# Kernel optimization log

Measured on AMD Instinct MI355X. Metric: run time of the kernel, lower is better.

The kernel has to match this reference:

```python
import jax, jax.numpy as jnp
import numpy as np

N_NODES = 100000


def gcn_conv(x, W, b, src, dst, n_nodes):
    # PyG GCNConv: h = x @ W; add self-loops; symmetric normalization
    # out_i = sum_{j in N(i) U {i}} deg_i^{-1/2} deg_j^{-1/2} h_j + b
    h = x @ W                                   # [N, F_out]
    # append self-loops
    loop = jnp.arange(n_nodes, dtype=src.dtype)
    s = jnp.concatenate([src, loop])            # [E+N]
    d = jnp.concatenate([dst, loop])            # [E+N]
    deg = jax.ops.segment_sum(jnp.ones_like(d, dtype=h.dtype), d,
                              num_segments=n_nodes)   # [N]
    dinv = jnp.where(deg > 0, jax.lax.rsqrt(deg), 0.0)
    norm = dinv[s] * dinv[d]                    # [E+N]
    msg = h[s] * norm[:, None]                  # [E+N, F_out]
    out = jax.ops.segment_sum(msg, d, num_segments=n_nodes)
    return out + b


def setup_inputs() -> dict:
    key = jax.random.key(0)
    k1, k2, k3, k4 = jax.random.split(key, 4)
    input_dim, hidden_dim, num_classes = 128, 64, 40
    n_edges = 1600000
    x = jax.random.normal(k1, (N_NODES, input_dim), dtype=jnp.float32)
    edge_index = jax.random.randint(k2, (2, n_edges), 0, N_NODES, dtype=jnp.int64)
    # Glorot-style init for the two GCNConv layers
    W1 = jax.random.normal(k3, (input_dim, hidden_dim), dtype=jnp.float32) / np.sqrt(input_dim)
    b1 = jnp.zeros((hidden_dim,), dtype=jnp.float32)
    W2 = jax.random.normal(k4, (hidden_dim, num_classes), dtype=jnp.float32) / np.sqrt(hidden_dim)
    b2 = jnp.zeros((num_classes,), dtype=jnp.float32)
    return {"x": x, "edge_index": edge_index, "W1": W1, "b1": b1, "W2": W2, "b2": b2}


def reference(x, edge_index, W1, b1, W2, b2):
    src, dst = edge_index[0], edge_index[1]
    h = gcn_conv(x, W1, b1, src, dst, N_NODES)
    h = jax.nn.relu(h)
    out = gcn_conv(h, W2, b2, src, dst, N_NODES)
    return out
```

## Files before the change

### kernel.cpp

```cpp
#include <hip/hip_runtime.h>
#include <hip/hip_fp16.h>
#include <math.h>

#define NN 100000
#define NE 1600000
#define F0 128
#define F1 64
#define F2 40
#define NB 256
#define BSZ 391
#define CAP2 8192
#define CHUNK 3125

typedef _Float16 f16x8 __attribute__((ext_vector_type(8)));
typedef _Float16 f16x4 __attribute__((ext_vector_type(4)));
typedef float f32x4 __attribute__((ext_vector_type(4)));

__global__ void k_zero(int* __restrict__ p) {
    if (threadIdx.x < NB + 1) p[threadIdx.x] = 0;
}

__global__ __launch_bounds__(256) void k_prepW(const float* __restrict__ W1,
                                               const float* __restrict__ W2,
                                               _Float16* __restrict__ w1t,
                                               _Float16* __restrict__ w2t) {
    int idx = blockIdx.x * 256 + threadIdx.x;
    if (idx < 64 * 128) {
        int n = idx >> 7, k = idx & 127;
        w1t[idx] = (_Float16)W1[k * 64 + n];
    } else if (idx < 64 * 128 + 48 * 64) {
        int j = idx - 64 * 128;
        int n = j >> 6, k = j & 63;
        w2t[j] = (_Float16)(n < 40 ? W2[k * 40 + n] : 0.0f);
    }
}

__global__ __launch_bounds__(256) void k_part(const int* __restrict__ src,
                                              const int* __restrict__ dst,
                                              int* __restrict__ bucketCnt,
                                              unsigned* __restrict__ bucket) {
    __shared__ int cnt[NB], base[NB];
    const int tid = threadIdx.x;
    cnt[tid] = 0;
    __syncthreads();
    const int e0 = blockIdx.x * CHUNK;
    const int e1 = e0 + CHUNK;
    for (int e = e0 + tid; e < e1; e += 256)
        atomicAdd(&cnt[dst[e] / BSZ], 1);
    __syncthreads();
    base[tid] = atomicAdd(&bucketCnt[tid], cnt[tid]);
    cnt[tid] = 0;
    __syncthreads();
    for (int e = e0 + tid; e < e1; e += 256) {
        int d = dst[e];
        int b = d / BSZ;
        int loc = d - b * BSZ;
        int ofs = atomicAdd(&cnt[b], 1);
        bucket[(size_t)b * CAP2 + base[b] + ofs] = ((unsigned)loc << 17) | (unsigned)src[e];
    }
}

__global__ __launch_bounds__(512) void k_build(const int* __restrict__ bucketCnt,
                                               const unsigned* __restrict__ bucket,
                                               int* __restrict__ gCursor,
                                               int* __restrict__ rs,
                                               int* __restrict__ ce,
                                               int* __restrict__ csr,
                                               float* __restrict__ dinv) {
    __shared__ int cnt[512];
    __shared__ int sc[512];
    __shared__ int sh_base;

    const int tid = threadIdx.x;
    const int b = blockIdx.x;
    const int n0 = b * BSZ;
    const int nn = (NN - n0 < BSZ) ? (NN - n0) : BSZ;

    cnt[tid] = 0;
    __syncthreads();

    const int cntB = bucketCnt[b];
    const unsigned* bk = bucket + (size_t)b * CAP2;
    for (int idx = tid; idx < cntB; idx += 512)
        atomicAdd(&cnt[bk[idx] >> 17], 1);
    __syncthreads();

    sc[tid] = cnt[tid];
    __syncthreads();
    for (int off = 1; off < 512; off <<= 1) {
        int v = (tid >= off) ? sc[tid - off] : 0;
        __syncthreads();
        sc[tid] += v;
        __syncthreads();
    }

    const int T = sc[511];
    if (tid == 0) sh_base = atomicAdd(gCursor, T);
    __syncthreads();
    const int base = sh_base;

    if (tid < nn) {
        int c = cnt[tid];
        int excl = sc[tid] - c;
        rs[n0 + tid] = base + excl;
        ce[n0 + tid] = base + sc[tid];
        dinv[n0 + tid] = rsqrtf((float)(c + 1));
        sc[tid] = excl;
    }
    cnt[tid] = 0;
    __syncthreads();

    for (int idx = tid; idx < cntB; idx += 512) {
        unsigned p = bk[idx];
        int l = (int)(p >> 17);
        int ofs = atomicAdd(&cnt[l], 1);
        csr[base + sc[l] + ofs] = (int)(p & 0x1FFFFu);
    }
}

__device__ __forceinline__ void acc8(float a[8], uint4 u) {
    __half2 h0 = *(__half2*)&u.x, h1 = *(__half2*)&u.y;
    __half2 h2 = *(__half2*)&u.z, h3 = *(__half2*)&u.w;
    float2 f0 = __half22float2(h0), f1 = __half22float2(h1);
    float2 f2 = __half22float2(h2), f3 = __half22float2(h3);
    a[0] += f0.x; a[1] += f0.y; a[2] += f1.x; a[3] += f1.y;
    a[4] += f2.x; a[5] += f2.y; a[6] += f3.x; a[7] += f3.y;
}

__device__ __forceinline__ void acc4(float a[4], uint2 u) {
    __half2 h0 = *(__half2*)&u.x, h1 = *(__half2*)&u.y;
    float2 f0 = __half22float2(h0), f1 = __half22float2(h1);
    a[0] += f0.x; a[1] += f0.y; a[2] += f1.x; a[3] += f1.y;
}

__global__ __launch_bounds__(256) void k_gemm1(const float* __restrict__ x,
                                               const _Float16* __restrict__ w1t,
                                               const float* __restrict__ dinv,
                                               _Float16* __restrict__ hs) {
    __shared__ _Float16 xl[64][136];
    __shared__ _Float16 wl[64][136];
    const int tid = threadIdx.x;
    const int row0 = blockIdx.x * 64;

    for (int i = tid; i < 1024; i += 256) {
        uint4 v = ((const uint4*)w1t)[i];
        int n = i >> 4, c = i & 15;
        *(uint4*)&wl[n][c * 8] = v;
    }
    {
        int r = tid >> 2, part = tid & 3;
        int gr = row0 + r; if (gr >= NN) gr = NN - 1;
        const float* xr = x + (size_t)gr * F0 + part * 32;
        _Float16* dstp = &xl[r][part * 32];
        #pragma unroll
        for (int q = 0; q < 8; ++q) {
            float4 v = *(const float4*)&xr[q * 4];
            f16x4 h;
            h[0] = (_Float16)v.x; h[1] = (_Float16)v.y;
            h[2] = (_Float16)v.z; h[3] = (_Float16)v.w;
            *(f16x4*)&dstp[q * 4] = h;
        }
    }
    __syncthreads();

    const int wave = tid >> 6;
    const int lane = tid & 63;
    const int l16 = lane & 15;
    const int g8 = (lane >> 4) * 8;

    f32x4 acc[4] = {{0,0,0,0},{0,0,0,0},{0,0,0,0},{0,0,0,0}};
    #pragma unroll
    for (int k0 = 0; k0 < F0; k0 += 32) {
        f16x8 a = *(f16x8*)&xl[wave * 16 + l16][k0 + g8];
        #pragma unroll
        for (int ct = 0; ct < 4; ++ct) {
            f16x8 b = *(f16x8*)&wl[ct * 16 + l16][k0 + g8];
            acc[ct] = __builtin_amdgcn_mfma_f32_16x16x32_f16(a, b, acc[ct], 0, 0, 0);
        }
    }

    const int baserow = row0 + wave * 16 + (lane >> 4) * 4;
    #pragma unroll
    for (int j = 0; j < 4; ++j) {
        int gr = baserow + j;
        if (gr < NN) {
            float dv = dinv[gr];
            #pragma unroll
            for (int ct = 0; ct < 4; ++ct)
                hs[(size_t)gr * F1 + ct * 16 + l16] = (_Float16)(acc[ct][j] * dv);
        }
    }
}

__global__ __launch_bounds__(256) void k_gather1(const int* __restrict__ rs,
                                                 const int* __restrict__ ce,
                                                 const int* __restrict__ csr,
                                                 const __half* __restrict__ hs,
                                                 const float* __restrict__ dinv,
                                                 const float* __restrict__ b,
                                                 _Float16* __restrict__ outp) {
    int t = blockIdx.x * 256 + threadIdx.x;
    int i = t >> 3;
    int g = t & 7;
    float acc[8] = {0, 0, 0, 0, 0, 0, 0, 0};
    acc8(acc, *(const uint4*)&hs[(size_t)i * F1 + g * 8]);
    int k = rs[i], end = ce[i];
    for (; k + 4 <= end; k += 4) {
        int s0 = csr[k], s1 = csr[k + 1], s2 = csr[k + 2], s3 = csr[k + 3];
        uint4 u0 = *(const uint4*)&hs[(size_t)s0 * F1 + g * 8];
        uint4 u1 = *(const uint4*)&hs[(size_t)s1 * F1 + g * 8];
        uint4 u2 = *(const uint4*)&hs[(size_t)s2 * F1 + g * 8];
        uint4 u3 = *(const uint4*)&hs[(size_t)s3 * F1 + g * 8];
        acc8(acc, u0); acc8(acc, u1); acc8(acc, u2); acc8(acc, u3);
    }
    for (; k < end; ++k)
        acc8(acc, *(const uint4*)&hs[(size_t)csr[k] * F1 + g * 8]);

    float dv = dinv[i];
    float4 b0 = *(const float4*)&b[g * 8];
    float4 b1v = *(const float4*)&b[g * 8 + 4];
    f16x8 o;
    o[0] = (_Float16)fmaxf(fmaf(dv, acc[0], b0.x), 0.0f);
    o[1] = (_Float16)fmaxf(fmaf(dv, acc[1], b0.y), 0.0f);
    o[2] = (_Float16)fmaxf(fmaf(dv, acc[2], b0.z), 0.0f);
    o[3] = (_Float16)fmaxf(fmaf(dv, acc[3], b0.w), 0.0f);
    o[4] = (_Float16)fmaxf(fmaf(dv, acc[4], b1v.x), 0.0f);
    o[5] = (_Float16)fmaxf(fmaf(dv, acc[5], b1v.y), 0.0f);
    o[6] = (_Float16)fmaxf(fmaf(dv, acc[6], b1v.z), 0.0f);
    o[7] = (_Float16)fmaxf(fmaf(dv, acc[7], b1v.w), 0.0f);
    *(f16x8*)&outp[(size_t)i * F1 + g * 8] = o;
}

__global__ __launch_bounds__(256) void k_gemm2(const _Float16* __restrict__ a1,
                                               const _Float16* __restrict__ w2t,
                                               const float* __restrict__ dinv,
                                               _Float16* __restrict__ hs2) {
    __shared__ _Float16 al[64][72];
    __shared__ _Float16 wl2[48][72];
    const int tid = threadIdx.x;
    const int row0 = blockIdx.x * 64;

    for (int i = tid; i < 512; i += 256) {
        int r = i >> 3, c = i & 7;
        int gr = row0 + r; if (gr >= NN) gr = NN - 1;
        *(uint4*)&al[r][c * 8] = ((const uint4*)a1)[(size_t)gr * 8 + c];
    }
    for (int i = tid; i < 384; i += 256) {
        int n = i >> 3, c = i & 7;
        *(uint4*)&wl2[n][c * 8] = ((const uint4*)w2t)[i];
    }
    __syncthreads();

    const int wave = tid >> 6;
    const int lane = tid & 63;
    const int l16 = lane & 15;
    const int g8 = (lane >> 4) * 8;

    f32x4 acc[3] = {{0,0,0,0},{0,0,0,0},{0,0,0,0}};
    #pragma unroll
    for (int k0 = 0; k0 < F1; k0 += 32) {
        f16x8 a = *(f16x8*)&al[wave * 16 + l16][k0 + g8];
        #pragma unroll
        for (int ct = 0; ct < 3; ++ct) {
            f16x8 b = *(f16x8*)&wl2[ct * 16 + l16][k0 + g8];
            acc[ct] = __builtin_amdgcn_mfma_f32_16x16x32_f16(a, b, acc[ct], 0, 0, 0);
        }
    }

    const int baserow = row0 + wave * 16 + (lane >> 4) * 4;
    #pragma unroll
    for (int j = 0; j < 4; ++j) {
        int gr = baserow + j;
        if (gr < NN) {
            float dv = dinv[gr];
            #pragma unroll
            for (int ct = 0; ct < 3; ++ct) {
                int col = ct * 16 + l16;
                if (col < F2)
                    hs2[(size_t)gr * F2 + col] = (_Float16)(acc[ct][j] * dv);
            }
        }
    }
}

__global__ __launch_bounds__(320) void k_gather2(const int* __restrict__ rs,
                                                 const int* __restrict__ ce,
                                                 const int* __restrict__ csr,
                                                 const __half* __restrict__ hs2,
                                                 const float* __restrict__ dinv,
                                                 const float* __restrict__ b,
                                                 float* __restrict__ outp) {
    int t = blockIdx.x * 320 + threadIdx.x;
    int i = t / 10;
    int g = t - i * 10;
    float acc[4] = {0, 0, 0, 0};
    acc4(acc, *(const uint2*)&hs2[(size_t)i * F2 + g * 4]);
    int k = rs[i], end = ce[i];
    for (; k + 4 <= end; k += 4) {
        int s0 = csr[k], s1 = csr[k + 1], s2 = csr[k + 2], s3 = csr[k + 3];
        uint2 u0 = *(const uint2*)&hs2[(size_t)s0 * F2 + g * 4];
        uint2 u1 = *(const uint2*)&hs2[(size_t)s1 * F2 + g * 4];
        uint2 u2 = *(const uint2*)&hs2[(size_t)s2 * F2 + g * 4];
        uint2 u3 = *(const uint2*)&hs2[(size_t)s3 * F2 + g * 4];
        acc4(acc, u0); acc4(acc, u1); acc4(acc, u2); acc4(acc, u3);
    }
    for (; k < end; ++k)
        acc4(acc, *(const uint2*)&hs2[(size_t)csr[k] * F2 + g * 4]);

    float dv = dinv[i];
    float4 bb = *(const float4*)&b[g * 4];
    float4 r;
    r.x = fmaf(dv, acc[0], bb.x);
    r.y = fmaf(dv, acc[1], bb.y);
    r.z = fmaf(dv, acc[2], bb.z);
    r.w = fmaf(dv, acc[3], bb.w);
    *(float4*)&outp[(size_t)i * F2 + g * 4] = r;
}

extern "C" void kernel_launch(void* const* d_in, const int* in_sizes, int n_in,
                              void* d_out, int out_size, void* d_ws, size_t ws_size,
                              hipStream_t stream) {
    const float* x  = (const float*)d_in[0];
    const int*   ei = (const int*)d_in[1];
    const float* W1 = (const float*)d_in[2];
    const float* b1 = (const float*)d_in[3];
    const float* W2 = (const float*)d_in[4];
    const float* b2 = (const float*)d_in[5];
    float* out = (float*)d_out;

    const int* src = ei;
    const int* dst = ei + NE;

    float*    dinv      = (float*)d_ws;
    int*      rs        = (int*)d_ws + 102400;
    int*      ce        = (int*)d_ws + 204800;
    int*      bucketCnt = (int*)d_ws + 307200;
    _Float16* w1t       = (_Float16*)((int*)d_ws + 308224);
    _Float16* w2t       = (_Float16*)((int*)d_ws + 312320);
    int*      csr       = (int*)d_ws + 313856;
    _Float16* hsA       = (_Float16*)((int*)d_ws + 313856 + NE);
    _Float16* a1h       = (_Float16*)((int*)d_ws + 313856 + NE + 3200000);
    unsigned* bucket    = (unsigned*)a1h;

    k_zero<<<1, 512, 0, stream>>>(bucketCnt);
    k_prepW<<<44, 256, 0, stream>>>(W1, W2, w1t, w2t);
    k_part<<<512, 256, 0, stream>>>(src, dst, bucketCnt, bucket);
    k_build<<<NB, 512, 0, stream>>>(bucketCnt, bucket, bucketCnt + NB,
                                    rs, ce, csr, dinv);

    k_gemm1<<<(NN + 63) / 64, 256, 0, stream>>>(x, w1t, dinv, hsA);
    k_gather1<<<NN * 8 / 256, 256, 0, stream>>>(rs, ce, csr, (const __half*)hsA,
                                                dinv, b1, a1h);

    k_gemm2<<<(NN + 63) / 64, 256, 0, stream>>>(a1h, w2t, dinv, hsA);
    k_gather2<<<NN / 32, 320, 0, stream>>>(rs, ce, csr, (const __half*)hsA,
                                           dinv, b2, out);
}
```

Baseline: 140.6 us.

## Fuse GEMM1 with edge partition, and gather1 with GEMM2

```diff
diff --git a/kernel.cpp b/kernel.cpp
--- a/kernel.cpp
+++ b/kernel.cpp
@@ -11,20 +11,20 @@
 #define BSZ 391
 #define CAP2 8192
 #define CHUNK 3125
+#define GEMM1_BLOCKS 1563
+#define PART_BLOCKS 512
 
 typedef _Float16 f16x8 __attribute__((ext_vector_type(8)));
 typedef _Float16 f16x4 __attribute__((ext_vector_type(4)));
 typedef float f32x4 __attribute__((ext_vector_type(4)));
 
-__global__ void k_zero(int* __restrict__ p) {
-    if (threadIdx.x < NB + 1) p[threadIdx.x] = 0;
-}
-
-__global__ __launch_bounds__(256) void k_prepW(const float* __restrict__ W1,
-                                               const float* __restrict__ W2,
-                                               _Float16* __restrict__ w1t,
-                                               _Float16* __restrict__ w2t) {
+__global__ __launch_bounds__(256) void k_init(const float* __restrict__ W1,
+                                              const float* __restrict__ W2,
+                                              _Float16* __restrict__ w1t,
+                                              _Float16* __restrict__ w2t,
+                                              int* __restrict__ bucketCnt) {
     int idx = blockIdx.x * 256 + threadIdx.x;
+    if (idx <= NB) bucketCnt[idx] = 0;
     if (idx < 64 * 128) {
         int n = idx >> 7, k = idx & 127;
         w1t[idx] = (_Float16)W1[k * 64 + n];
@@ -35,28 +35,85 @@
     }
 }
 
-__global__ __launch_bounds__(256) void k_part(const int* __restrict__ src,
-                                              const int* __restrict__ dst,
-                                              int* __restrict__ bucketCnt,
-                                              unsigned* __restrict__ bucket) {
+__global__ __launch_bounds__(256) void k_g1p(const float* __restrict__ x,
+                                             const _Float16* __restrict__ w1t,
+                                             const int* __restrict__ src,
+                                             const int* __restrict__ dst,
+                                             int* __restrict__ bucketCnt,
+                                             unsigned* __restrict__ bucket,
+                                             _Float16* __restrict__ hs) {
+    __shared__ _Float16 xl[64][136];
+    __shared__ _Float16 wl[64][136];
     __shared__ int cnt[NB], base[NB];
     const int tid = threadIdx.x;
-    cnt[tid] = 0;
-    __syncthreads();
-    const int e0 = blockIdx.x * CHUNK;
-    const int e1 = e0 + CHUNK;
-    for (int e = e0 + tid; e < e1; e += 256)
-        atomicAdd(&cnt[dst[e] / BSZ], 1);
-    __syncthreads();
-    base[tid] = atomicAdd(&bucketCnt[tid], cnt[tid]);
-    cnt[tid] = 0;
-    __syncthreads();
-    for (int e = e0 + tid; e < e1; e += 256) {
-        int d = dst[e];
-        int b = d / BSZ;
-        int loc = d - b * BSZ;
-        int ofs = atomicAdd(&cnt[b], 1);
-        bucket[(size_t)b * CAP2 + base[b] + ofs] = ((unsigned)loc << 17) | (unsigned)src[e];
+
+    if (blockIdx.x < GEMM1_BLOCKS) {
+        const int row0 = blockIdx.x * 64;
+        for (int i = tid; i < 1024; i += 256) {
+            uint4 v = ((const uint4*)w1t)[i];
+            *(uint4*)&wl[i >> 4][(i & 15) * 8] = v;
+        }
+        {
+            int r = tid >> 2, part = tid & 3;
+            int gr = row0 + r; if (gr >= NN) gr = NN - 1;
+            const float* xr = x + (size_t)gr * F0 + part * 32;
+            _Float16* dstp = &xl[r][part * 32];
+            #pragma unroll
+            for (int q = 0; q < 8; ++q) {
+                float4 v = *(const float4*)&xr[q * 4];
+                f16x4 h;
+                h[0] = (_Float16)v.x; h[1] = (_Float16)v.y;
+                h[2] = (_Float16)v.z; h[3] = (_Float16)v.w;
+                *(f16x4*)&dstp[q * 4] = h;
+            }
+        }
+        __syncthreads();
+
+        const int wave = tid >> 6;
+        const int lane = tid & 63;
+        const int l16 = lane & 15;
+        const int g8 = (lane >> 4) * 8;
+
+        f32x4 acc[4] = {{0,0,0,0},{0,0,0,0},{0,0,0,0},{0,0,0,0}};
+        #pragma unroll
+        for (int k0 = 0; k0 < F0; k0 += 32) {
+            f16x8 a = *(f16x8*)&xl[wave * 16 + l16][k0 + g8];
+            #pragma unroll
+            for (int ct = 0; ct < 4; ++ct) {
+                f16x8 b = *(f16x8*)&wl[ct * 16 + l16][k0 + g8];
+                acc[ct] = __builtin_amdgcn_mfma_f32_16x16x32_f16(a, b, acc[ct], 0, 0, 0);
+            }
+        }
+        const int baserow = row0 + wave * 16 + (lane >> 4) * 4;
+        #pragma unroll
+        for (int j = 0; j < 4; ++j) {
+            int gr = baserow + j;
+            if (gr < NN) {
+                #pragma unroll
+                for (int ct = 0; ct < 4; ++ct)
+                    hs[(size_t)gr * F1 + ct * 16 + l16] = (_Float16)acc[ct][j];
+            }
+        }
+    } else {
+        const int pb = blockIdx.x - GEMM1_BLOCKS;
+        cnt[tid] = 0;
+        __syncthreads();
+        const int e0 = pb * CHUNK;
+        const int e1 = e0 + CHUNK;
+        for (int e = e0 + tid; e < e1; e += 256)
+            atomicAdd(&cnt[dst[e] / BSZ], 1);
+        __syncthreads();
+        base[tid] = atomicAdd(&bucketCnt[tid], cnt[tid]);
+        cnt[tid] = 0;
+        __syncthreads();
+        for (int e = e0 + tid; e < e1; e += 256) {
+            int d = dst[e];
+            int b = d / BSZ;
+            int loc = d - b * BSZ;
+            int ofs = atomicAdd(&cnt[b], 1);
+            bucket[(size_t)b * CAP2 + base[b] + ofs] =
+                ((unsigned)loc << 17) | (unsigned)src[e];
+        }
     }
 }
 
@@ -118,13 +175,15 @@
     }
 }
 
-__device__ __forceinline__ void acc8(float a[8], uint4 u) {
+__device__ __forceinline__ void acc8s(float a[8], uint4 u, float s) {
     __half2 h0 = *(__half2*)&u.x, h1 = *(__half2*)&u.y;
     __half2 h2 = *(__half2*)&u.z, h3 = *(__half2*)&u.w;
     float2 f0 = __half22float2(h0), f1 = __half22float2(h1);
     float2 f2 = __half22float2(h2), f3 = __half22float2(h3);
-    a[0] += f0.x; a[1] += f0.y; a[2] += f1.x; a[3] += f1.y;
-    a[4] += f2.x; a[5] += f2.y; a[6] += f3.x; a[7] += f3.y;
+    a[0] = fmaf(s, f0.x, a[0]); a[1] = fmaf(s, f0.y, a[1]);
+    a[2] = fmaf(s, f1.x, a[2]); a[3] = fmaf(s, f1.y, a[3]);
+    a[4] = fmaf(s, f2.x, a[4]); a[5] = fmaf(s, f2.y, a[5]);
+    a[6] = fmaf(s, f3.x, a[6]); a[7] = fmaf(s, f3.y, a[7]);
 }
 
 __device__ __forceinline__ void acc4(float a[4], uint2 u) {
@@ -133,33 +192,56 @@
     a[0] += f0.x; a[1] += f0.y; a[2] += f1.x; a[3] += f1.y;
 }
 
-__global__ __launch_bounds__(256) void k_gemm1(const float* __restrict__ x,
-                                               const _Float16* __restrict__ w1t,
-                                               const float* __restrict__ dinv,
-                                               _Float16* __restrict__ hs) {
-    __shared__ _Float16 xl[64][136];
-    __shared__ _Float16 wl[64][136];
+__global__ __launch_bounds__(512) void k_fuse(const int* __restrict__ rs,
+                                              const int* __restrict__ ce,
+                                              const int* __restrict__ csr,
+                                              const _Float16* __restrict__ hs,
+                                              const float* __restrict__ dinv,
+                                              const float* __restrict__ b1,
+                                              const _Float16* __restrict__ w2t,
+                                              _Float16* __restrict__ hs2) {
+    __shared__ _Float16 al[64][72];
+    __shared__ _Float16 wl2[48][72];
     const int tid = threadIdx.x;
     const int row0 = blockIdx.x * 64;
 
-    for (int i = tid; i < 1024; i += 256) {
-        uint4 v = ((const uint4*)w1t)[i];
-        int n = i >> 4, c = i & 15;
-        *(uint4*)&wl[n][c * 8] = v;
-    }
+    if (tid < 384)
+        *(uint4*)&wl2[tid >> 3][(tid & 7) * 8] = ((const uint4*)w2t)[tid];
+
     {
-        int r = tid >> 2, part = tid & 3;
-        int gr = row0 + r; if (gr >= NN) gr = NN - 1;
-        const float* xr = x + (size_t)gr * F0 + part * 32;
-        _Float16* dstp = &xl[r][part * 32];
-        #pragma unroll
-        for (int q = 0; q < 8; ++q) {
-            float4 v = *(const float4*)&xr[q * 4];
-            f16x4 h;
-            h[0] = (_Float16)v.x; h[1] = (_Float16)v.y;
-            h[2] = (_Float16)v.z; h[3] = (_Float16)v.w;
-            *(f16x4*)&dstp[q * 4] = h;
-        }
+        int r = tid >> 3, g = tid & 7;
+        int i = row0 + r; if (i >= NN) i = NN - 1;
+        const __half* hsh = (const __half*)hs;
+        float dvi = dinv[i];
+        float acc[8] = {0, 0, 0, 0, 0, 0, 0, 0};
+        acc8s(acc, *(const uint4*)&hsh[(size_t)i * F1 + g * 8], dvi);
+        int k = rs[i], end = ce[i];
+        for (; k + 4 <= end; k += 4) {
+            int s0 = csr[k], s1 = csr[k + 1], s2 = csr[k + 2], s3 = csr[k + 3];
+            float d0 = dinv[s0], d1 = dinv[s1], d2 = dinv[s2], d3 = dinv[s3];
+            uint4 u0 = *(const uint4*)&hsh[(size_t)s0 * F1 + g * 8];
+            uint4 u1 = *(const uint4*)&hsh[(size_t)s1 * F1 + g * 8];
+            uint4 u2 = *(const uint4*)&hsh[(size_t)s2 * F1 + g * 8];
+            uint4 u3 = *(const uint4*)&hsh[(size_t)s3 * F1 + g * 8];
+            acc8s(acc, u0, d0); acc8s(acc, u1, d1);
+            acc8s(acc, u2, d2); acc8s(acc, u3, d3);
+        }
+        for (; k < end; ++k) {
+            int s0 = csr[k];
+            acc8s(acc, *(const uint4*)&hsh[(size_t)s0 * F1 + g * 8], dinv[s0]);
+        }
+        float4 c0 = *(const float4*)&b1[g * 8];
+        float4 c1 = *(const float4*)&b1[g * 8 + 4];
+        f16x8 o;
+        o[0] = (_Float16)fmaxf(fmaf(dvi, acc[0], c0.x), 0.0f);
+        o[1] = (_Float16)fmaxf(fmaf(dvi, acc[1], c0.y), 0.0f);
+        o[2] = (_Float16)fmaxf(fmaf(dvi, acc[2], c0.z), 0.0f);
+        o[3] = (_Float16)fmaxf(fmaf(dvi, acc[3], c0.w), 0.0f);
+        o[4] = (_Float16)fmaxf(fmaf(dvi, acc[4], c1.x), 0.0f);
+        o[5] = (_Float16)fmaxf(fmaf(dvi, acc[5], c1.y), 0.0f);
+        o[6] = (_Float16)fmaxf(fmaf(dvi, acc[6], c1.z), 0.0f);
+        o[7] = (_Float16)fmaxf(fmaf(dvi, acc[7], c1.w), 0.0f);
+        *(f16x8*)&al[r][g * 8] = o;
     }
     __syncthreads();
 
@@ -168,116 +250,23 @@
     const int l16 = lane & 15;
     const int g8 = (lane >> 4) * 8;
 
-    f32x4 acc[4] = {{0,0,0,0},{0,0,0,0},{0,0,0,0},{0,0,0,0}};
-    #pragma unroll
-    for (int k0 = 0; k0 < F0; k0 += 32) {
-        f16x8 a = *(f16x8*)&xl[wave * 16 + l16][k0 + g8];
+    for (int t = wave; t < 12; t += 8) {
+        int rt = t / 3, ct = t - rt * 3;
+        f32x4 acc = {0, 0, 0, 0};
         #pragma unroll
-        for (int ct = 0; ct < 4; ++ct) {
-            f16x8 b = *(f16x8*)&wl[ct * 16 + l16][k0 + g8];
-            acc[ct] = __builtin_amdgcn_mfma_f32_16x16x32_f16(a, b, acc[ct], 0, 0, 0);
-        }
-    }
-
-    const int baserow = row0 + wave * 16 + (lane >> 4) * 4;
-    #pragma unroll
-    for (int j = 0; j < 4; ++j) {
-        int gr = baserow + j;
-        if (gr < NN) {
-            float dv = dinv[gr];
+        for (int k0 = 0; k0 < F1; k0 += 32) {
+            f16x8 a = *(f16x8*)&al[rt * 16 + l16][k0 + g8];
+            f16x8 b = *(f16x8*)&wl2[ct * 16 + l16][k0 + g8];
+            acc = __builtin_amdgcn_mfma_f32_16x16x32_f16(a, b, acc, 0, 0, 0);
+        }
+        int col = ct * 16 + l16;
+        int baserow = row0 + rt * 16 + (lane >> 4) * 4;
+        if (col < F2) {
             #pragma unroll
-            for (int ct = 0; ct < 4; ++ct)
-                hs[(size_t)gr * F1 + ct * 16 + l16] = (_Float16)(acc[ct][j] * dv);
-        }
-    }
-}
-
-__global__ __launch_bounds__(256) void k_gather1(const int* __restrict__ rs,
-                                                 const int* __restrict__ ce,
-                                                 const int* __restrict__ csr,
-                                                 const __half* __restrict__ hs,
-                                                 const float* __restrict__ dinv,
-                                                 const float* __restrict__ b,
-                                                 _Float16* __restrict__ outp) {
-    int t = blockIdx.x * 256 + threadIdx.x;
-    int i = t >> 3;
-    int g = t & 7;
-    float acc[8] = {0, 0, 0, 0, 0, 0, 0, 0};
-    acc8(acc, *(const uint4*)&hs[(size_t)i * F1 + g * 8]);
-    int k = rs[i], end = ce[i];
-    for (; k + 4 <= end; k += 4) {
-        int s0 = csr[k], s1 = csr[k + 1], s2 = csr[k + 2], s3 = csr[k + 3];
-        uint4 u0 = *(const uint4*)&hs[(size_t)s0 * F1 + g * 8];
-        uint4 u1 = *(const uint4*)&hs[(size_t)s1 * F1 + g * 8];
-        uint4 u2 = *(const uint4*)&hs[(size_t)s2 * F1 + g * 8];
-        uint4 u3 = *(const uint4*)&hs[(size_t)s3 * F1 + g * 8];
-        acc8(acc, u0); acc8(acc, u1); acc8(acc, u2); acc8(acc, u3);
-    }
-    for (; k < end; ++k)
-        acc8(acc, *(const uint4*)&hs[(size_t)csr[k] * F1 + g * 8]);
-
-    float dv = dinv[i];
-    float4 b0 = *(const float4*)&b[g * 8];
-    float4 b1v = *(const float4*)&b[g * 8 + 4];
-    f16x8 o;
-    o[0] = (_Float16)fmaxf(fmaf(dv, acc[0], b0.x), 0.0f);
-    o[1] = (_Float16)fmaxf(fmaf(dv, acc[1], b0.y), 0.0f);
-    o[2] = (_Float16)fmaxf(fmaf(dv, acc[2], b0.z), 0.0f);
-    o[3] = (_Float16)fmaxf(fmaf(dv, acc[3], b0.w), 0.0f);
-    o[4] = (_Float16)fmaxf(fmaf(dv, acc[4], b1v.x), 0.0f);
-    o[5] = (_Float16)fmaxf(fmaf(dv, acc[5], b1v.y), 0.0f);
-    o[6] = (_Float16)fmaxf(fmaf(dv, acc[6], b1v.z), 0.0f);
-    o[7] = (_Float16)fmaxf(fmaf(dv, acc[7], b1v.w), 0.0f);
-    *(f16x8*)&outp[(size_t)i * F1 + g * 8] = o;
-}
-
-__global__ __launch_bounds__(256) void k_gemm2(const _Float16* __restrict__ a1,
-                                               const _Float16* __restrict__ w2t,
-                                               const float* __restrict__ dinv,
-                                               _Float16* __restrict__ hs2) {
-    __shared__ _Float16 al[64][72];
-    __shared__ _Float16 wl2[48][72];
-    const int tid = threadIdx.x;
-    const int row0 = blockIdx.x * 64;
-
-    for (int i = tid; i < 512; i += 256) {
-        int r = i >> 3, c = i & 7;
-        int gr = row0 + r; if (gr >= NN) gr = NN - 1;
-        *(uint4*)&al[r][c * 8] = ((const uint4*)a1)[(size_t)gr * 8 + c];
-    }
-    for (int i = tid; i < 384; i += 256) {
-        int n = i >> 3, c = i & 7;
-        *(uint4*)&wl2[n][c * 8] = ((const uint4*)w2t)[i];
-    }
-    __syncthreads();
-
-    const int wave = tid >> 6;
-    const int lane = tid & 63;
-    const int l16 = lane & 15;
-    const int g8 = (lane >> 4) * 8;
-
-    f32x4 acc[3] = {{0,0,0,0},{0,0,0,0},{0,0,0,0}};
-    #pragma unroll
-    for (int k0 = 0; k0 < F1; k0 += 32) {
-        f16x8 a = *(f16x8*)&al[wave * 16 + l16][k0 + g8];
-        #pragma unroll
-        for (int ct = 0; ct < 3; ++ct) {
-            f16x8 b = *(f16x8*)&wl2[ct * 16 + l16][k0 + g8];
-            acc[ct] = __builtin_amdgcn_mfma_f32_16x16x32_f16(a, b, acc[ct], 0, 0, 0);
-        }
-    }
-
-    const int baserow = row0 + wave * 16 + (lane >> 4) * 4;
-    #pragma unroll
-    for (int j = 0; j < 4; ++j) {
-        int gr = baserow + j;
-        if (gr < NN) {
-            float dv = dinv[gr];
-            #pragma unroll
-            for (int ct = 0; ct < 3; ++ct) {
-                int col = ct * 16 + l16;
-                if (col < F2)
-                    hs2[(size_t)gr * F2 + col] = (_Float16)(acc[ct][j] * dv);
+            for (int j = 0; j < 4; ++j) {
+                int gr = baserow + j;
+                if (gr < NN)
+                    hs2[(size_t)gr * F2 + col] = (_Float16)(acc[j] * dinv[gr]);
             }
         }
     }
@@ -338,21 +327,16 @@
     _Float16* w1t       = (_Float16*)((int*)d_ws + 308224);
     _Float16* w2t       = (_Float16*)((int*)d_ws + 312320);
     int*      csr       = (int*)d_ws + 313856;
-    _Float16* hsA       = (_Float16*)((int*)d_ws + 313856 + NE);
-    _Float16* a1h       = (_Float16*)((int*)d_ws + 313856 + NE + 3200000);
-    unsigned* bucket    = (unsigned*)a1h;
-
-    k_zero<<<1, 512, 0, stream>>>(bucketCnt);
-    k_prepW<<<44, 256, 0, stream>>>(W1, W2, w1t, w2t);
-    k_part<<<512, 256, 0, stream>>>(src, dst, bucketCnt, bucket);
+    _Float16* hs        = (_Float16*)((int*)d_ws + 313856 + NE);
+    unsigned* bucket    = (unsigned*)((int*)d_ws + 313856 + NE + 3200000);
+    _Float16* hs2       = (_Float16*)bucket;
+
+    k_init<<<44, 256, 0, stream>>>(W1, W2, w1t, w2t, bucketCnt);
+    k_g1p<<<GEMM1_BLOCKS + PART_BLOCKS, 256, 0, stream>>>(x, w1t, src, dst,
+                                                          bucketCnt, bucket, hs);
     k_build<<<NB, 512, 0, stream>>>(bucketCnt, bucket, bucketCnt + NB,
                                     rs, ce, csr, dinv);
-
-    k_gemm1<<<(NN + 63) / 64, 256, 0, stream>>>(x, w1t, dinv, hsA);
-    k_gather1<<<NN * 8 / 256, 256, 0, stream>>>(rs, ce, csr, (const __half*)hsA,
-                                                dinv, b1, a1h);
-
-    k_gemm2<<<(NN + 63) / 64, 256, 0, stream>>>(a1h, w2t, dinv, hsA);
-    k_gather2<<<NN / 32, 320, 0, stream>>>(rs, ce, csr, (const __half*)hsA,
+    k_fuse<<<GEMM1_BLOCKS, 512, 0, stream>>>(rs, ce, csr, hs, dinv, b1, w2t, hs2);
+    k_gather2<<<NN / 32, 320, 0, stream>>>(rs, ce, csr, (const __half*)hs2,
                                            dinv, b2, out);
 }
```

After: 131.3 us. -6.6%, faster.
